# Kernel tuning notes

Hardware: AMD Instinct MI355X
Metric: run time of the kernel (lower is better)

## Reference

```python
import jax, jax.numpy as jnp
import numpy as np

N = 100000   # nodes
E = 1600000  # edges
F = 128      # in_feats
H = 4        # heads
D = 32       # out_feats per head
NEG_SLOPE = 0.2


def setup_inputs() -> dict:
    key = jax.random.key(0)
    k1, k2, k3, k4, k5, k6 = jax.random.split(key, 6)
    feat = jax.random.normal(k1, (N, F), dtype=jnp.float32)
    W = jax.random.normal(k2, (H * D, F), dtype=jnp.float32) * (1.0 / np.sqrt(F))
    attn_l = jax.random.normal(k3, (1, H, D), dtype=jnp.float32) * 0.1
    attn_r = jax.random.normal(k4, (1, H, D), dtype=jnp.float32) * 0.1
    src = jax.random.randint(k5, (E,), 0, N, dtype=jnp.int32)
    dst = jax.random.randint(k6, (E,), 0, N, dtype=jnp.int32)
    return {"feat": feat, "W": W, "attn_l": attn_l, "attn_r": attn_r, "src": src, "dst": dst}


def reference(feat, W, attn_l, attn_r, src, dst):
    # fc projection: [N, F] -> [N, H, D]
    h = (feat @ W.T).reshape(N, H, D)
    # per-node attention logits [N, H]
    el = jnp.sum(h * attn_l, axis=-1)
    er = jnp.sum(h * attn_r, axis=-1)
    # edge scores: el[src] + er[dst] -> leaky relu  [E, H]
    e = jax.nn.leaky_relu(el[src] + er[dst], negative_slope=NEG_SLOPE)
    # segment softmax over edges grouped by destination node, per head
    m = jax.ops.segment_max(e, dst, num_segments=N)          # [N, H]
    ex = jnp.exp(e - m[dst])                                 # [E, H]
    s = jax.ops.segment_sum(ex, dst, num_segments=N)         # [N, H]
    alpha = ex / s[dst]                                      # [E, H]
    # weighted sparse aggregation: out[dst] += alpha * h[src]
    msgs = alpha[:, :, None] * h[src]                        # [E, H, D]
    rst = jax.ops.segment_sum(msgs, dst, num_segments=N)     # [N, H, D]
    return rst
```

## Files before the change

kernel.cpp:

```cpp
#include <hip/hip_runtime.h>

constexpr int N_NODES = 100000;
constexpr int E_EDGES = 1600000;
constexpr int NBLK    = (N_NODES + 1023) / 1024;

typedef _Float16 f16;
typedef _Float16 f16x2 __attribute__((ext_vector_type(2)));
typedef _Float16 f16x8 __attribute__((ext_vector_type(8)));
typedef float f32x4 __attribute__((ext_vector_type(4)));

__global__ __launch_bounds__(256, 2) void k_gemm(const float* __restrict__ feat,
                                                 const float* __restrict__ W,
                                                 const float* __restrict__ attn_l,
                                                 const float* __restrict__ attn_r,
                                                 f16* __restrict__ h2,
                                                 float* __restrict__ el,
                                                 float* __restrict__ er) {
    __shared__ f16 Wlds[128 * 128];
    char* wb = (char*)Wlds;
    const int tid = threadIdx.x;

    {
        int n = tid >> 1;
        int kh = (tid & 1) * 64;
        const float* wsrc = W + n * 128 + kh;
#pragma unroll
        for (int q = 0; q < 8; ++q) {
            float4 u0 = *reinterpret_cast<const float4*>(wsrc + q * 8);
            float4 u1 = *reinterpret_cast<const float4*>(wsrc + q * 8 + 4);
            f16x8 v;
            v[0] = (f16)u0.x; v[1] = (f16)u0.y; v[2] = (f16)u0.z; v[3] = (f16)u0.w;
            v[4] = (f16)u1.x; v[5] = (f16)u1.y; v[6] = (f16)u1.z; v[7] = (f16)u1.w;
            unsigned byte = (unsigned)(n * 256 + kh * 2 + q * 16) ^ ((n & 7) << 4);
            *reinterpret_cast<f16x8*>(wb + byte) = v;
        }
    }
    __syncthreads();

    const int wav  = tid >> 6;
    const int lane = tid & 63;
    const int la = lane & 15;
    const int lb = lane >> 4;
    const int row0w = blockIdx.x * 64 + wav * 16;

    f16x8 afrag[4];
    {
        int rowA = row0w + la;
        if (rowA >= N_NODES) rowA = N_NODES - 1;
        const float* ap = feat + (size_t)rowA * 128 + lb * 8;
#pragma unroll
        for (int kk = 0; kk < 4; ++kk) {
            float4 u0 = *reinterpret_cast<const float4*>(ap + kk * 32);
            float4 u1 = *reinterpret_cast<const float4*>(ap + kk * 32 + 4);
            f16x8 a;
            a[0] = (f16)u0.x; a[1] = (f16)u0.y; a[2] = (f16)u0.z; a[3] = (f16)u0.w;
            a[4] = (f16)u1.x; a[5] = (f16)u1.y; a[6] = (f16)u1.z; a[7] = (f16)u1.w;
            afrag[kk] = a;
        }
    }

    f32x4 acc[8];
#pragma unroll
    for (int t = 0; t < 8; ++t) acc[t] = (f32x4){0.f, 0.f, 0.f, 0.f};

#pragma unroll
    for (int t = 0; t < 8; ++t) {
        int col = t * 16 + la;
#pragma unroll
        for (int kk = 0; kk < 4; ++kk) {
            unsigned byte = (unsigned)(col * 256 + (kk * 32 + lb * 8) * 2) ^ ((col & 7) << 4);
            f16x8 b = *reinterpret_cast<const f16x8*>(wb + byte);
            acc[t] = __builtin_amdgcn_mfma_f32_16x16x32_f16(afrag[kk], b, acc[t], 0, 0, 0);
        }
    }

#pragma unroll
    for (int t = 0; t < 8; ++t) {
#pragma unroll
        for (int r = 0; r < 4; ++r) {
            int row = row0w + lb * 4 + r;
            if (row < N_NODES) h2[(size_t)row * 128 + t * 16 + la] = (f16)acc[t][r];
        }
    }

    float elp[4][4], erp[4][4];
#pragma unroll
    for (int r = 0; r < 4; ++r)
#pragma unroll
        for (int g = 0; g < 4; ++g) { elp[r][g] = 0.f; erp[r][g] = 0.f; }

#pragma unroll
    for (int t = 0; t < 8; ++t) {
        float alv = attn_l[t * 16 + la];
        float arv = attn_r[t * 16 + la];
        int g = t >> 1;
#pragma unroll
        for (int r = 0; r < 4; ++r) {
            elp[r][g] += acc[t][r] * alv;
            erp[r][g] += acc[t][r] * arv;
        }
    }
#pragma unroll
    for (int r = 0; r < 4; ++r)
#pragma unroll
        for (int g = 0; g < 4; ++g) {
            float v = elp[r][g];
            v += __shfl_xor(v, 1, 64); v += __shfl_xor(v, 2, 64);
            v += __shfl_xor(v, 4, 64); v += __shfl_xor(v, 8, 64);
            elp[r][g] = v;
            float u = erp[r][g];
            u += __shfl_xor(u, 1, 64); u += __shfl_xor(u, 2, 64);
            u += __shfl_xor(u, 4, 64); u += __shfl_xor(u, 8, 64);
            erp[r][g] = u;
        }
    if (la == 0) {
#pragma unroll
        for (int r = 0; r < 4; ++r) {
            int row = row0w + lb * 4 + r;
            if (row < N_NODES) {
                *reinterpret_cast<float4*>(el + (size_t)row * 4) =
                    make_float4(elp[r][0], elp[r][1], elp[r][2], elp[r][3]);
                *reinterpret_cast<float4*>(er + (size_t)row * 4) =
                    make_float4(erp[r][0], erp[r][1], erp[r][2], erp[r][3]);
            }
        }
    }
}

__global__ void k_hist(const int* __restrict__ dst, int* __restrict__ deg,
                       int* __restrict__ rank) {
    int e = blockIdx.x * blockDim.x + threadIdx.x;
    if (e < E_EDGES) rank[e] = atomicAdd(&deg[dst[e]], 1);
}

__global__ void k_bsum(const int* __restrict__ deg, int* __restrict__ aux) {
    int tid = threadIdx.x;
    int i0 = blockIdx.x * 1024 + tid * 4;
    int sum = 0;
#pragma unroll
    for (int j = 0; j < 4; ++j)
        if (i0 + j < N_NODES) sum += deg[i0 + j];
#pragma unroll
    for (int m = 32; m; m >>= 1) sum += __shfl_xor(sum, m, 64);
    __shared__ int wsums[4];
    if ((tid & 63) == 0) wsums[tid >> 6] = sum;
    __syncthreads();
    if (tid == 0) aux[blockIdx.x] = wsums[0] + wsums[1] + wsums[2] + wsums[3];
}

__global__ void k_scanaux(int* __restrict__ aux) {
    __shared__ int s[128];
    int i = threadIdx.x;
    int v = (i < NBLK) ? aux[i] : 0;
    s[i] = v;
    __syncthreads();
#pragma unroll
    for (int d = 1; d < 128; d <<= 1) {
        int t = (i >= d) ? s[i - d] : 0;
        __syncthreads();
        s[i] += t;
        __syncthreads();
    }
    if (i < NBLK) aux[i] = s[i] - v;
}

__global__ void k_bscan(const int* __restrict__ deg, const int* __restrict__ aux,
                        int* __restrict__ start) {
    int tid = threadIdx.x;
    int lane = tid & 63;
    int wid = tid >> 6;
    int i0 = blockIdx.x * 1024 + tid * 4;
    int v[4];
#pragma unroll
    for (int j = 0; j < 4; ++j)
        v[j] = (i0 + j < N_NODES) ? deg[i0 + j] : 0;
    int tsum = v[0] + v[1] + v[2] + v[3];
    int x = tsum;
#pragma unroll
    for (int d = 1; d < 64; d <<= 1) {
        int t = __shfl_up(x, d, 64);
        if (lane >= d) x += t;
    }
    __shared__ int wsums[4];
    if (lane == 63) wsums[wid] = x;
    __syncthreads();
    int base = aux[blockIdx.x];
#pragma unroll
    for (int w = 0; w < 4; ++w)
        if (w < wid) base += wsums[w];
    int p = base + x - tsum;
#pragma unroll
    for (int j = 0; j < 4; ++j) {
        if (i0 + j < N_NODES) start[i0 + j] = p;
        p += v[j];
    }
}

__global__ void k_scatter(const int* __restrict__ src, const int* __restrict__ dst,
                          const int* __restrict__ rank, const int* __restrict__ start,
                          int* __restrict__ ssrc) {
    int e = blockIdx.x * blockDim.x + threadIdx.x;
    if (e < E_EDGES) ssrc[start[dst[e]] + rank[e]] = src[e];
}

__global__ __launch_bounds__(256) void k_aggr(const f16* __restrict__ h2,
                                              const float* __restrict__ el,
                                              const float* __restrict__ er,
                                              const int* __restrict__ ssrc,
                                              const int* __restrict__ start,
                                              const int* __restrict__ deg,
                                              float* __restrict__ out) {
    int n = blockIdx.x * 4 + (threadIdx.x >> 6);
    int lane = threadIdx.x & 63;
    int g = lane >> 4;
    int d = deg[n];
    int s0 = start[n];
    float ern = er[n * 4 + g];

    f16x2 ac0 = {0, 0}, ac1 = {0, 0}, ac2 = {0, 0}, ac3 = {0, 0};
    f16x2 sw0 = {0, 0}, sw1 = {0, 0}, sw2 = {0, 0}, sw3 = {0, 0};

    for (int i = 0; i < d; i += 4) {
        bool v1 = (i + 1) < d, v2 = (i + 2) < d, v3 = (i + 3) < d;
        int n0 = ssrc[s0 + i];
        int n1 = ssrc[s0 + (v1 ? i + 1 : 0)];
        int n2 = ssrc[s0 + (v2 ? i + 2 : 0)];
        int n3 = ssrc[s0 + (v3 ? i + 3 : 0)];
        float e0 = el[n0 * 4 + g];
        float e1 = el[n1 * 4 + g];
        float e2 = el[n2 * 4 + g];
        float e3 = el[n3 * 4 + g];
        f16x2 q0 = reinterpret_cast<const f16x2*>(h2 + (size_t)n0 * 128)[lane];
        f16x2 q1 = reinterpret_cast<const f16x2*>(h2 + (size_t)n1 * 128)[lane];
        f16x2 q2 = reinterpret_cast<const f16x2*>(h2 + (size_t)n2 * 128)[lane];
        f16x2 q3 = reinterpret_cast<const f16x2*>(h2 + (size_t)n3 * 128)[lane];

        float x0 = e0 + ern; x0 = fmaxf(x0, 0.2f * x0);
        float x1 = e1 + ern; x1 = fmaxf(x1, 0.2f * x1);
        float x2 = e2 + ern; x2 = fmaxf(x2, 0.2f * x2);
        float x3 = e3 + ern; x3 = fmaxf(x3, 0.2f * x3);
        float w0 = __expf(x0);
        float w1 = v1 ? __expf(x1) : 0.f;
        float w2 = v2 ? __expf(x2) : 0.f;
        float w3 = v3 ? __expf(x3) : 0.f;

        f16 h0 = (f16)w0; f16x2 wv0 = {h0, h0};
        f16 h1 = (f16)w1; f16x2 wv1 = {h1, h1};
        f16 h2w = (f16)w2; f16x2 wv2 = {h2w, h2w};
        f16 h3 = (f16)w3; f16x2 wv3 = {h3, h3};

        ac0 += wv0 * q0; sw0 += wv0;
        ac1 += wv1 * q1; sw1 += wv1;
        ac2 += wv2 * q2; sw2 += wv2;
        ac3 += wv3 * q3; sw3 += wv3;
    }

    f16x2 ac = (ac0 + ac1) + (ac2 + ac3);
    f16x2 sw = (sw0 + sw1) + (sw2 + sw3);
    float swf = (float)sw[0];
    float inv = (d > 0) ? 1.0f / swf : 0.0f;
    float2 o = make_float2((float)ac[0] * inv, (float)ac[1] * inv);
    reinterpret_cast<float2*>(out + (size_t)n * 128)[lane] = o;
}

extern "C" void kernel_launch(void* const* d_in, const int* in_sizes, int n_in,
                              void* d_out, int out_size, void* d_ws, size_t ws_size,
                              hipStream_t stream) {
    const float* feat   = (const float*)d_in[0];
    const float* W      = (const float*)d_in[1];
    const float* attn_l = (const float*)d_in[2];
    const float* attn_r = (const float*)d_in[3];
    const int*   src    = (const int*)d_in[4];
    const int*   dst    = (const int*)d_in[5];
    float* out = (float*)d_out;

    f16*   h2    = (f16*)d_ws;
    float* el    = (float*)(h2 + (size_t)N_NODES * 128);
    float* er    = el + (size_t)N_NODES * 4;
    int*   deg   = (int*)(er + (size_t)N_NODES * 4);
    int*   start = deg + N_NODES;
    int*   rank  = start + N_NODES;
    int*   ssrc  = rank + E_EDGES;
    int*   aux   = ssrc + E_EDGES;

    hipMemsetAsync(deg, 0, N_NODES * sizeof(int), stream);

    k_hist<<<(E_EDGES + 255) / 256, 256, 0, stream>>>(dst, deg, rank);
    k_gemm<<<(N_NODES + 63) / 64, 256, 0, stream>>>(feat, W, attn_l, attn_r, h2, el, er);
    k_bsum<<<NBLK, 256, 0, stream>>>(deg, aux);
    k_scanaux<<<1, 128, 0, stream>>>(aux);
    k_bscan<<<NBLK, 256, 0, stream>>>(deg, aux, start);
    k_scatter<<<(E_EDGES + 255) / 256, 256, 0, stream>>>(src, dst, rank, start, ssrc);
    k_aggr<<<N_NODES / 4, 256, 0, stream>>>(h2, el, er, ssrc, start, deg, out);
}
```

Before: 215.1 us.

## Fuse histogram into GEMM launch, pad CSR segments to four with dummy node

The degree histogram now runs as extra blocks of the GEMM kernel, with each thread handling four edges through int4 loads, which removes one launch and lets the two overlap. CSR segments are padded to multiples of four and filled with a sentinel node whose feature row is zero and whose el logit is very negative. This lets the aggregation loop drop its per-edge validity predicates and clamped index reads. The aggregation kernel also moves to 128-thread blocks and reads the segment start with readfirstlane. The cost is a slightly larger workspace and extra padding writes in the scan kernel.

```diff
diff --git a/kernel.cpp b/kernel.cpp
--- a/kernel.cpp
+++ b/kernel.cpp
@@ -3,23 +3,37 @@
 constexpr int N_NODES = 100000;
 constexpr int E_EDGES = 1600000;
 constexpr int NBLK    = (N_NODES + 1023) / 1024;
+constexpr int GEMM_BLOCKS = (N_NODES + 63) / 64;
+constexpr int HIST_BLOCKS = (E_EDGES / 4 + 255) / 256;
 
 typedef _Float16 f16;
 typedef _Float16 f16x2 __attribute__((ext_vector_type(2)));
 typedef _Float16 f16x8 __attribute__((ext_vector_type(8)));
 typedef float f32x4 __attribute__((ext_vector_type(4)));
 
-__global__ __launch_bounds__(256, 2) void k_gemm(const float* __restrict__ feat,
-                                                 const float* __restrict__ W,
-                                                 const float* __restrict__ attn_l,
-                                                 const float* __restrict__ attn_r,
-                                                 f16* __restrict__ h2,
-                                                 float* __restrict__ el,
-                                                 float* __restrict__ er) {
+__global__ __launch_bounds__(256, 2) void k_gemm_hist(
+        const float* __restrict__ feat, const float* __restrict__ W,
+        const float* __restrict__ attn_l, const float* __restrict__ attn_r,
+        f16* __restrict__ h2, float* __restrict__ el, float* __restrict__ er,
+        const int4* __restrict__ dst4, int* __restrict__ deg,
+        int4* __restrict__ rank4) {
     __shared__ f16 Wlds[128 * 128];
+
+    if (blockIdx.x >= GEMM_BLOCKS) {
+        int t = (blockIdx.x - GEMM_BLOCKS) * 256 + threadIdx.x;
+        if (t < E_EDGES / 4) {
+            int4 d = dst4[t];
+            int r0 = atomicAdd(&deg[d.x], 1);
+            int r1 = atomicAdd(&deg[d.y], 1);
+            int r2 = atomicAdd(&deg[d.z], 1);
+            int r3 = atomicAdd(&deg[d.w], 1);
+            rank4[t] = make_int4(r0, r1, r2, r3);
+        }
+        return;
+    }
+
     char* wb = (char*)Wlds;
     const int tid = threadIdx.x;
-
     {
         int n = tid >> 1;
         int kh = (tid & 1) * 64;
@@ -127,19 +141,13 @@
     }
 }
 
-__global__ void k_hist(const int* __restrict__ dst, int* __restrict__ deg,
-                       int* __restrict__ rank) {
-    int e = blockIdx.x * blockDim.x + threadIdx.x;
-    if (e < E_EDGES) rank[e] = atomicAdd(&deg[dst[e]], 1);
-}
-
 __global__ void k_bsum(const int* __restrict__ deg, int* __restrict__ aux) {
     int tid = threadIdx.x;
     int i0 = blockIdx.x * 1024 + tid * 4;
     int sum = 0;
 #pragma unroll
     for (int j = 0; j < 4; ++j)
-        if (i0 + j < N_NODES) sum += deg[i0 + j];
+        if (i0 + j < N_NODES) sum += (deg[i0 + j] + 3) & ~3;
 #pragma unroll
     for (int m = 32; m; m >>= 1) sum += __shfl_xor(sum, m, 64);
     __shared__ int wsums[4];
@@ -165,16 +173,27 @@
 }
 
 __global__ void k_bscan(const int* __restrict__ deg, const int* __restrict__ aux,
-                        int* __restrict__ start) {
+                        int* __restrict__ start, int* __restrict__ ssrc,
+                        f16* __restrict__ h2, float* __restrict__ el) {
+    if (blockIdx.x == 0 && threadIdx.x == 0) {
+        float4 z = make_float4(0.f, 0.f, 0.f, 0.f);
+        float4* hrow = reinterpret_cast<float4*>(h2 + (size_t)N_NODES * 128);
+#pragma unroll
+        for (int q = 0; q < 16; ++q) hrow[q] = z;
+        *reinterpret_cast<float4*>(el + (size_t)N_NODES * 4) =
+            make_float4(-1e4f, -1e4f, -1e4f, -1e4f);
+    }
     int tid = threadIdx.x;
     int lane = tid & 63;
     int wid = tid >> 6;
     int i0 = blockIdx.x * 1024 + tid * 4;
-    int v[4];
-#pragma unroll
-    for (int j = 0; j < 4; ++j)
-        v[j] = (i0 + j < N_NODES) ? deg[i0 + j] : 0;
-    int tsum = v[0] + v[1] + v[2] + v[3];
+    int v[4], pv[4];
+#pragma unroll
+    for (int j = 0; j < 4; ++j) {
+        v[j]  = (i0 + j < N_NODES) ? deg[i0 + j] : 0;
+        pv[j] = (v[j] + 3) & ~3;
+    }
+    int tsum = pv[0] + pv[1] + pv[2] + pv[3];
     int x = tsum;
 #pragma unroll
     for (int d = 1; d < 64; d <<= 1) {
@@ -191,8 +210,11 @@
     int p = base + x - tsum;
 #pragma unroll
     for (int j = 0; j < 4; ++j) {
-        if (i0 + j < N_NODES) start[i0 + j] = p;
-        p += v[j];
+        if (i0 + j < N_NODES) {
+            start[i0 + j] = p;
+            for (int q = v[j]; q < pv[j]; ++q) ssrc[p + q] = N_NODES;
+        }
+        p += pv[j];
     }
 }
 
@@ -203,33 +225,34 @@
     if (e < E_EDGES) ssrc[start[dst[e]] + rank[e]] = src[e];
 }
 
-__global__ __launch_bounds__(256) void k_aggr(const f16* __restrict__ h2,
+__global__ __launch_bounds__(128) void k_aggr(const f16* __restrict__ h2,
                                               const float* __restrict__ el,
                                               const float* __restrict__ er,
                                               const int* __restrict__ ssrc,
                                               const int* __restrict__ start,
                                               const int* __restrict__ deg,
                                               float* __restrict__ out) {
-    int n = blockIdx.x * 4 + (threadIdx.x >> 6);
+    int n = blockIdx.x * 2 + (threadIdx.x >> 6);
+    if (n >= N_NODES) return;
     int lane = threadIdx.x & 63;
     int g = lane >> 4;
     int d = deg[n];
-    int s0 = start[n];
+    int pd = (d + 3) & ~3;
+    int s0 = __builtin_amdgcn_readfirstlane(start[n]);
     float ern = er[n * 4 + g];
 
     f16x2 ac0 = {0, 0}, ac1 = {0, 0}, ac2 = {0, 0}, ac3 = {0, 0};
     f16x2 sw0 = {0, 0}, sw1 = {0, 0}, sw2 = {0, 0}, sw3 = {0, 0};
 
-    for (int i = 0; i < d; i += 4) {
-        bool v1 = (i + 1) < d, v2 = (i + 2) < d, v3 = (i + 3) < d;
+    for (int i = 0; i < pd; i += 4) {
         int n0 = ssrc[s0 + i];
-        int n1 = ssrc[s0 + (v1 ? i + 1 : 0)];
-        int n2 = ssrc[s0 + (v2 ? i + 2 : 0)];
-        int n3 = ssrc[s0 + (v3 ? i + 3 : 0)];
-        float e0 = el[n0 * 4 + g];
-        float e1 = el[n1 * 4 + g];
-        float e2 = el[n2 * 4 + g];
-        float e3 = el[n3 * 4 + g];
+        int n1 = ssrc[s0 + i + 1];
+        int n2 = ssrc[s0 + i + 2];
+        int n3 = ssrc[s0 + i + 3];
+        float e0 = el[(size_t)n0 * 4 + g];
+        float e1 = el[(size_t)n1 * 4 + g];
+        float e2 = el[(size_t)n2 * 4 + g];
+        float e3 = el[(size_t)n3 * 4 + g];
         f16x2 q0 = reinterpret_cast<const f16x2*>(h2 + (size_t)n0 * 128)[lane];
         f16x2 q1 = reinterpret_cast<const f16x2*>(h2 + (size_t)n1 * 128)[lane];
         f16x2 q2 = reinterpret_cast<const f16x2*>(h2 + (size_t)n2 * 128)[lane];
@@ -240,14 +263,14 @@
         float x2 = e2 + ern; x2 = fmaxf(x2, 0.2f * x2);
         float x3 = e3 + ern; x3 = fmaxf(x3, 0.2f * x3);
         float w0 = __expf(x0);
-        float w1 = v1 ? __expf(x1) : 0.f;
-        float w2 = v2 ? __expf(x2) : 0.f;
-        float w3 = v3 ? __expf(x3) : 0.f;
-
-        f16 h0 = (f16)w0; f16x2 wv0 = {h0, h0};
-        f16 h1 = (f16)w1; f16x2 wv1 = {h1, h1};
-        f16 h2w = (f16)w2; f16x2 wv2 = {h2w, h2w};
-        f16 h3 = (f16)w3; f16x2 wv3 = {h3, h3};
+        float w1 = __expf(x1);
+        float w2 = __expf(x2);
+        float w3 = __expf(x3);
+
+        f16 a0 = (f16)w0; f16x2 wv0 = {a0, a0};
+        f16 a1 = (f16)w1; f16x2 wv1 = {a1, a1};
+        f16 a2 = (f16)w2; f16x2 wv2 = {a2, a2};
+        f16 a3 = (f16)w3; f16x2 wv3 = {a3, a3};
 
         ac0 += wv0 * q0; sw0 += wv0;
         ac1 += wv1 * q1; sw1 += wv1;
@@ -275,21 +298,21 @@
     float* out = (float*)d_out;
 
     f16*   h2    = (f16*)d_ws;
-    float* el    = (float*)(h2 + (size_t)N_NODES * 128);
-    float* er    = el + (size_t)N_NODES * 4;
+    float* el    = (float*)(h2 + (size_t)(N_NODES + 8) * 128);
+    float* er    = el + (size_t)(N_NODES + 4) * 4;
     int*   deg   = (int*)(er + (size_t)N_NODES * 4);
     int*   start = deg + N_NODES;
     int*   rank  = start + N_NODES;
     int*   ssrc  = rank + E_EDGES;
-    int*   aux   = ssrc + E_EDGES;
+    int*   aux   = ssrc + E_EDGES + 3 * N_NODES + 64;
 
     hipMemsetAsync(deg, 0, N_NODES * sizeof(int), stream);
 
-    k_hist<<<(E_EDGES + 255) / 256, 256, 0, stream>>>(dst, deg, rank);
-    k_gemm<<<(N_NODES + 63) / 64, 256, 0, stream>>>(feat, W, attn_l, attn_r, h2, el, er);
+    k_gemm_hist<<<GEMM_BLOCKS + HIST_BLOCKS, 256, 0, stream>>>(
+        feat, W, attn_l, attn_r, h2, el, er, (const int4*)dst, deg, (int4*)rank);
     k_bsum<<<NBLK, 256, 0, stream>>>(deg, aux);
     k_scanaux<<<1, 128, 0, stream>>>(aux);
-    k_bscan<<<NBLK, 256, 0, stream>>>(deg, aux, start);
+    k_bscan<<<NBLK, 256, 0, stream>>>(deg, aux, start, ssrc, h2, el);
     k_scatter<<<(E_EDGES + 255) / 256, 256, 0, stream>>>(src, dst, rank, start, ssrc);
-    k_aggr<<<N_NODES / 4, 256, 0, stream>>>(h2, el, er, ssrc, start, deg, out);
-}
+    k_aggr<<<(N_NODES + 1) / 2, 128, 0, stream>>>(h2, el, er, ssrc, start, deg, out);
+}
```

After: 211.5 us. Within noise of the previous version (-1.7%).
